# Performance work log

Measured on AMD Instinct MI355X. Metric: run time of the kernel, lower is better.

The kernel has to match this reference:

```python
import jax, jax.numpy as jnp
import numpy as np

T = 4        # number of atom types (len(atomtype))
N = 65536    # number of atoms
D = 256      # nl[0] == nl[1] == nl[2]
EPS = 1e-5   # LayerNorm eps (torch default)


def setup_inputs() -> dict:
    key = jax.random.key(0)
    ks = jax.random.split(key, 16)
    s = 1.0 / np.sqrt(D)  # xavier-ish scale
    f32 = jnp.float32
    return {
        "density": jax.random.normal(ks[0], (N, D), f32),
        "species": jax.random.randint(ks[1], (N,), 0, T, jnp.int32),
        # first Linear(nl[0], nl[1]) per type
        "W0": jax.random.normal(ks[2], (T, D, D), f32) * s,
        "b0": jnp.zeros((T, D), f32),
        # ResBlock: actfun (Relu_like: alpha*silu(Wx+b)), LayerNorm, Linear
        "Wa": jax.random.normal(ks[3], (T, D, D), f32) * s,
        "ba": jnp.zeros((T, D), f32),
        "alpha_a": jnp.ones((T, D), f32),
        "gamma": jnp.ones((T, D), f32),
        "beta_ln": jnp.zeros((T, D), f32),
        "Wl": jax.random.normal(ks[4], (T, D, D), f32) * s,
        "bl": jnp.zeros((T, D), f32),
        # tail actfun(nl[nhid-1], nl[nhid])
        "Wf": jax.random.normal(ks[5], (T, D, D), f32) * s,
        "bf": jnp.zeros((T, D), f32),
        "alpha_f": jnp.ones((T, D), f32),
        # output Linear(nl[nhid], outputneuron=1); randomized (zero-init is degenerate for testing)
        "Wo": jax.random.normal(ks[6], (T, 1, D), f32) * s,
        "bo": jnp.zeros((T, 1), f32),
    }


def _layernorm(x, g, b):
    mu = jnp.mean(x, axis=-1, keepdims=True)
    var = jnp.mean((x - mu) ** 2, axis=-1, keepdims=True)
    return g * (x - mu) * jax.lax.rsqrt(var + EPS) + b


def _expert(W0, b0, Wa, ba, alpha_a, gamma, beta_ln, Wl, bl, Wf, bf, alpha_f, Wo, bo, density):
    # Sequential: Linear -> ResBlock(actfun, LN, Linear) -> actfun -> Linear
    x = density @ W0.T + b0                       # [N, D]
    h = alpha_a * jax.nn.silu(x @ Wa.T + ba)      # Relu_like actfun
    h = _layernorm(h, gamma, beta_ln)
    x = x + (h @ Wl.T + bl)                       # residual add
    x = alpha_f * jax.nn.silu(x @ Wf.T + bf)
    return x @ Wo.T + bo                          # [N, 1]


def reference(density, species, W0, b0, Wa, ba, alpha_a, gamma, beta_ln, Wl, bl, Wf, bf, alpha_f, Wo, bo):
    # Apply every type's expert to all atoms, then pick the row for each atom's type.
    # Same math as the torch gather/scatter dispatch (every species value is in [0, T)).
    y_all = jax.vmap(_expert, in_axes=(0,) * 14 + (None,))(
        W0, b0, Wa, ba, alpha_a, gamma, beta_ln, Wl, bl, Wf, bf, alpha_f, Wo, bo, density
    )  # [T, N, 1]
    return y_all[species, jnp.arange(N)]          # [N, 1]
```

## Files before the change

kernel.cpp:

```cpp
#include <hip/hip_runtime.h>
#include <hip/hip_bf16.h>


#define D 256
#define T 4
#define MT 64
#define NTHREADS 256
#define LDSTRIDE 264

typedef __attribute__((ext_vector_type(8))) short bf16x8;
typedef __attribute__((ext_vector_type(4))) float f32x4;

__device__ __forceinline__ float bf2f(unsigned short s) {
    union { unsigned u; float f; } c;
    c.u = ((unsigned)s) << 16;
    return c.f;
}
__device__ __forceinline__ unsigned short f2bf(float f) {
    union { float f; unsigned u; } c;
    c.f = f;
    unsigned u = c.u;
    u += 0x7fffu + ((u >> 16) & 1u);
    return (unsigned short)(u >> 16);
}
__device__ __forceinline__ unsigned pack2(float a, float b) {
    return (unsigned)f2bf(a) | ((unsigned)f2bf(b) << 16);
}
__device__ __forceinline__ float lo2f(unsigned u) { return bf2f((unsigned short)(u & 0xffffu)); }
__device__ __forceinline__ float hi2f(unsigned u) { return bf2f((unsigned short)(u >> 16)); }
__device__ __forceinline__ float silu(float v) { return v / (1.f + __expf(-v)); }


extern "C" __global__ void k_hist(const int* __restrict__ species, int* counts, int N,
                                  const float* __restrict__ s0, const float* __restrict__ s1,
                                  const float* __restrict__ s2, const float* __restrict__ s3,
                                  unsigned short* __restrict__ d0, unsigned short* __restrict__ d1,
                                  unsigned short* __restrict__ d2, unsigned short* __restrict__ d3, int n4) {
    __shared__ int h[T];
    int tid = threadIdx.x;
    if (tid < T) h[tid] = 0;
    __syncthreads();
    int i = blockIdx.x * blockDim.x + tid;
    if (i < N) atomicAdd(&h[species[i]], 1);
    __syncthreads();
    if (tid < T) atomicAdd(&counts[tid], h[tid]);
    if (i < n4) {
        float4 v;
        v = ((const float4*)s0)[i];
        ((ushort4*)d0)[i] = make_ushort4(f2bf(v.x), f2bf(v.y), f2bf(v.z), f2bf(v.w));
        v = ((const float4*)s1)[i];
        ((ushort4*)d1)[i] = make_ushort4(f2bf(v.x), f2bf(v.y), f2bf(v.z), f2bf(v.w));
        v = ((const float4*)s2)[i];
        ((ushort4*)d2)[i] = make_ushort4(f2bf(v.x), f2bf(v.y), f2bf(v.z), f2bf(v.w));
        v = ((const float4*)s3)[i];
        ((ushort4*)d3)[i] = make_ushort4(f2bf(v.x), f2bf(v.y), f2bf(v.z), f2bf(v.w));
    }
}

extern "C" __global__ void k_scatter(const int* __restrict__ species, const int* __restrict__ counts,
                                     int* cursors, int* __restrict__ perm, int N) {
    __shared__ int lh[T], lbase[T];
    int tid = threadIdx.x;
    if (tid < T) lh[tid] = 0;
    __syncthreads();
    int i = blockIdx.x * blockDim.x + tid;
    int t = (i < N) ? species[i] : -1;
    int rank = 0;
    if (t >= 0) rank = atomicAdd(&lh[t], 1);
    __syncthreads();
    if (tid < T) lbase[tid] = atomicAdd(&cursors[tid], lh[tid]);
    __syncthreads();
    if (t >= 0) {
        int off = 0;
        for (int j = 0; j < t; ++j) off += counts[j];
        perm[off + lbase[t] + rank] = i;
    }
}


extern "C" __global__ void __launch_bounds__(NTHREADS, 2)
fused_moe(const float* __restrict__ density,
          const int* __restrict__ perm,
          const int* __restrict__ counts,
          const unsigned short* __restrict__ W0b,
          const unsigned short* __restrict__ Wab,
          const unsigned short* __restrict__ Wlb,
          const unsigned short* __restrict__ Wfb,
          const float* __restrict__ b0g, const float* __restrict__ bag,
          const float* __restrict__ aag, const float* __restrict__ gg,
          const float* __restrict__ btg, const float* __restrict__ blg,
          const float* __restrict__ bfg, const float* __restrict__ afg,
          const float* __restrict__ Wog, const float* __restrict__ bog,
          float* __restrict__ out, int N)
{
    __shared__ unsigned short Xs[MT * LDSTRIDE];
    __shared__ float Pb0[D], Pba[D], Paa[D], Pg[D], Pbt[D], Pbl[D], Pbf[D], Paf[D], Pwo[D];
    __shared__ float red1[NTHREADS], red2[NTHREADS];
    __shared__ float muS[MT], rsS[MT];

    const int tid = threadIdx.x;

    int c[T];
#pragma unroll
    for (int i = 0; i < T; ++i) c[i] = counts[i];
    int t = -1, tile = 0, rem = blockIdx.x, off = 0;
#pragma unroll
    for (int i = 0; i < T; ++i) {
        int ti = (c[i] + MT - 1) >> 6;
        if (t < 0) {
            if (rem < ti) { t = i; tile = rem; }
            else { rem -= ti; off += c[i]; }
        }
    }
    if (t < 0) return;
    const int bstart = off + tile * MT;
    const int nrows = min(MT, c[t] - tile * MT);

    {
        int j = t * D + tid;
        Pb0[tid] = b0g[j]; Pba[tid] = bag[j]; Paa[tid] = aag[j];
        Pg[tid]  = gg[j];  Pbt[tid] = btg[j]; Pbl[tid] = blg[j];
        Pbf[tid] = bfg[j]; Paf[tid] = afg[j]; Pwo[tid] = Wog[j];
    }

#pragma unroll
    for (int p = 0; p < 4; ++p) {
        int row = p * 16 + (tid >> 4);
        int cbase = (tid & 15) * 4;
        unsigned short* dst = Xs + row * LDSTRIDE;
        if (row < nrows) {
            const float* src = density + (size_t)perm[bstart + row] * D;
#pragma unroll
            for (int j = 0; j < 4; ++j) {
                int col = cbase + j * 64;
                float4 v = *(const float4*)(src + col);
                *(ushort4*)(dst + col) = make_ushort4(f2bf(v.x), f2bf(v.y), f2bf(v.z), f2bf(v.w));
            }
        } else {
#pragma unroll
            for (int j = 0; j < 4; ++j) {
                int col = cbase + j * 64;
                *(ushort4*)(dst + col) = make_ushort4(0, 0, 0, 0);
            }
        }
    }
    __syncthreads();

    const int lane = tid & 63;
    const int w    = tid >> 6;
    const int ml   = lane & 15;
    const int qk   = (lane >> 4) * 8;
    const int qr   = (lane >> 4) * 4;

    const size_t wmat = (size_t)t * D * D;
    const unsigned short* W0t = W0b + wmat;
    const unsigned short* Wat = Wab + wmat;
    const unsigned short* Wlt = Wlb + wmat;
    const unsigned short* Wft = Wfb + wmat;

    f32x4 acc[4][4];
    const f32x4 zero4 = {0.f, 0.f, 0.f, 0.f};

    auto do_gemm = [&](const unsigned short* __restrict__ W) {
#pragma unroll
        for (int mi = 0; mi < 4; ++mi)
#pragma unroll
            for (int ni = 0; ni < 4; ++ni) acc[mi][ni] = zero4;
#pragma unroll
        for (int k0 = 0; k0 < D; k0 += 32) {
            bf16x8 a[4], b[4];
#pragma unroll
            for (int mi = 0; mi < 4; ++mi)
                a[mi] = *(const bf16x8*)(W + (size_t)(w * 64 + mi * 16 + ml) * D + k0 + qk);
#pragma unroll
            for (int ni = 0; ni < 4; ++ni)
                b[ni] = *(const bf16x8*)(Xs + (ni * 16 + ml) * LDSTRIDE + k0 + qk);
#pragma unroll
            for (int mi = 0; mi < 4; ++mi)
#pragma unroll
                for (int ni = 0; ni < 4; ++ni)
                    acc[mi][ni] = __builtin_amdgcn_mfma_f32_16x16x32_bf16(a[mi], b[ni], acc[mi][ni], 0, 0, 0);
        }
    };


    do_gemm(W0t);
    __syncthreads();
    unsigned res[4][4][2];
#pragma unroll
    for (int mi = 0; mi < 4; ++mi) {
#pragma unroll
        for (int ni = 0; ni < 4; ++ni) {
            int r0 = w * 64 + mi * 16 + qr;
            int a0 = ni * 16 + ml;
            float4 bb = *(const float4*)(Pb0 + r0);
            float v0 = acc[mi][ni][0] + bb.x;
            float v1 = acc[mi][ni][1] + bb.y;
            float v2 = acc[mi][ni][2] + bb.z;
            float v3 = acc[mi][ni][3] + bb.w;
            res[mi][ni][0] = pack2(v0, v1);
            res[mi][ni][1] = pack2(v2, v3);
            *(ushort4*)(Xs + a0 * LDSTRIDE + r0) =
                make_ushort4(f2bf(v0), f2bf(v1), f2bf(v2), f2bf(v3));
        }
    }
    __syncthreads();

    do_gemm(Wat);
    __syncthreads();
#pragma unroll
    for (int mi = 0; mi < 4; ++mi) {
#pragma unroll
        for (int ni = 0; ni < 4; ++ni) {
            int r0 = w * 64 + mi * 16 + qr;
            int a0 = ni * 16 + ml;
            float4 bb = *(const float4*)(Pba + r0);
            float4 aa = *(const float4*)(Paa + r0);
            float v0 = aa.x * silu(acc[mi][ni][0] + bb.x);
            float v1 = aa.y * silu(acc[mi][ni][1] + bb.y);
            float v2 = aa.z * silu(acc[mi][ni][2] + bb.z);
            float v3 = aa.w * silu(acc[mi][ni][3] + bb.w);
            *(ushort4*)(Xs + a0 * LDSTRIDE + r0) =
                make_ushort4(f2bf(v0), f2bf(v1), f2bf(v2), f2bf(v3));
        }
    }
    __syncthreads();

    {
        int row = tid & 63, q = tid >> 6;
        const bf16x8* base = (const bf16x8*)(Xs + row * LDSTRIDE + q * 64);
        bf16x8 hv[8];
        float sum = 0.f, ssq = 0.f;
#pragma unroll
        for (int j = 0; j < 8; ++j) {
            hv[j] = base[j];
#pragma unroll
            for (int e = 0; e < 8; ++e) {
                float f = bf2f((unsigned short)hv[j][e]);
                sum += f; ssq += f * f;
            }
        }
        red1[tid] = sum; red2[tid] = ssq;
        __syncthreads();
        if (tid < MT) {
            float s  = red1[tid] + red1[tid + 64] + red1[tid + 128] + red1[tid + 192];
            float sq = red2[tid] + red2[tid + 64] + red2[tid + 128] + red2[tid + 192];
            float mu = s * (1.f / D);
            float var = sq * (1.f / D) - mu * mu;
            muS[tid] = mu;
            rsS[tid] = rsqrtf(var + 1e-5f);
        }
        __syncthreads();
        float mu = muS[row], rs = rsS[row];
        bf16x8* wbase = (bf16x8*)(Xs + row * LDSTRIDE + q * 64);
#pragma unroll
        for (int j = 0; j < 8; ++j) {
            bf16x8 o;
#pragma unroll
            for (int e = 0; e < 8; ++e) {
                int col = q * 64 + j * 8 + e;
                float f = bf2f((unsigned short)hv[j][e]);
                o[e] = (short)f2bf(Pg[col] * (f - mu) * rs + Pbt[col]);
            }
            wbase[j] = o;
        }
    }
    __syncthreads();

    do_gemm(Wlt);
    __syncthreads();
#pragma unroll
    for (int mi = 0; mi < 4; ++mi) {
#pragma unroll
        for (int ni = 0; ni < 4; ++ni) {
            int r0 = w * 64 + mi * 16 + qr;
            int a0 = ni * 16 + ml;
            float4 bb = *(const float4*)(Pbl + r0);
            float v0 = acc[mi][ni][0] + bb.x + lo2f(res[mi][ni][0]);
            float v1 = acc[mi][ni][1] + bb.y + hi2f(res[mi][ni][0]);
            float v2 = acc[mi][ni][2] + bb.z + lo2f(res[mi][ni][1]);
            float v3 = acc[mi][ni][3] + bb.w + hi2f(res[mi][ni][1]);
            *(ushort4*)(Xs + a0 * LDSTRIDE + r0) =
                make_ushort4(f2bf(v0), f2bf(v1), f2bf(v2), f2bf(v3));
        }
    }
    __syncthreads();

    do_gemm(Wft);
    __syncthreads();
#pragma unroll
    for (int mi = 0; mi < 4; ++mi) {
#pragma unroll
        for (int ni = 0; ni < 4; ++ni) {
            int r0 = w * 64 + mi * 16 + qr;
            int a0 = ni * 16 + ml;
            float4 bb = *(const float4*)(Pbf + r0);
            float4 aa = *(const float4*)(Paf + r0);
            float v0 = aa.x * silu(acc[mi][ni][0] + bb.x);
            float v1 = aa.y * silu(acc[mi][ni][1] + bb.y);
            float v2 = aa.z * silu(acc[mi][ni][2] + bb.z);
            float v3 = aa.w * silu(acc[mi][ni][3] + bb.w);
            *(ushort4*)(Xs + a0 * LDSTRIDE + r0) =
                make_ushort4(f2bf(v0), f2bf(v1), f2bf(v2), f2bf(v3));
        }
    }
    __syncthreads();

    {
        int row = tid & 63, q = tid >> 6;
        const bf16x8* base = (const bf16x8*)(Xs + row * LDSTRIDE + q * 64);
        float part = 0.f;
#pragma unroll
        for (int j = 0; j < 8; ++j) {
            bf16x8 hv = base[j];
#pragma unroll
            for (int e = 0; e < 8; ++e)
                part += bf2f((unsigned short)hv[e]) * Pwo[q * 64 + j * 8 + e];
        }
        red1[tid] = part;
        __syncthreads();
        if (tid < nrows) {
            float val = red1[tid] + red1[tid + 64] + red1[tid + 128] + red1[tid + 192] + bog[t];
            out[perm[bstart + tid]] = val;
        }
    }
}


extern "C" void kernel_launch(void* const* d_in, const int* in_sizes, int n_in,
                              void* d_out, int out_size, void* d_ws, size_t ws_size,
                              hipStream_t stream) {
    const float* density = (const float*)d_in[0];
    const int*   species = (const int*)d_in[1];
    const float* W0      = (const float*)d_in[2];
    const float* b0      = (const float*)d_in[3];
    const float* Wa      = (const float*)d_in[4];
    const float* ba      = (const float*)d_in[5];
    const float* alpha_a = (const float*)d_in[6];
    const float* gamma   = (const float*)d_in[7];
    const float* beta_ln = (const float*)d_in[8];
    const float* Wl      = (const float*)d_in[9];
    const float* bl      = (const float*)d_in[10];
    const float* Wf      = (const float*)d_in[11];
    const float* bfv     = (const float*)d_in[12];
    const float* alpha_f = (const float*)d_in[13];
    const float* Wo      = (const float*)d_in[14];
    const float* bo      = (const float*)d_in[15];
    float* out = (float*)d_out;
    const int N = in_sizes[1];

    char* ws = (char*)d_ws;
    int* counts  = (int*)ws;
    int* cursors = (int*)(ws + 16);
    int* perm    = (int*)(ws + 64);
    const size_t wsz = (size_t)T * D * D;
    unsigned short* W0b = (unsigned short*)(ws + 64 + (size_t)N * 4);
    unsigned short* Wab = W0b + wsz;
    unsigned short* Wlb = Wab + wsz;
    unsigned short* Wfb = Wlb + wsz;

    hipMemsetAsync(ws, 0, 32, stream);
    int n4 = (int)(wsz / 4);
    k_hist<<<(N + 255) / 256, 256, 0, stream>>>(species, counts, N, W0, Wa, Wl, Wf,
                                                W0b, Wab, Wlb, Wfb, n4);
    k_scatter<<<(N + 255) / 256, 256, 0, stream>>>(species, counts, cursors, perm, N);

    int nblocks = (N + MT - 1) / MT + T;
    fused_moe<<<nblocks, NTHREADS, 0, stream>>>(density, perm, counts, W0b, Wab, Wlb, Wfb,
                                                b0, ba, alpha_a, gamma, beta_ln, bl, bfv, alpha_f,
                                                Wo, bo, out, N);
}
```

Measured before the change: 223.1 us.

## Merge histogram and scatter into one prep kernel with per-type bucket buffers

The separate histogram and scatter kernels are replaced by a single prep kernel. It uses wavefront ballot/popcount to rank atoms within each species and appends them to fixed per-type buckets of size N, so prefix offsets from a prior count pass are no longer needed. The final cursors serve as counts for the main kernel. It also swaps the manual bf16 rounding for the hardware v_cvt_pk_bf16_f32 instruction, uses rcp in silu, and reuses two LDS parameter arrays to cut shared memory. The cost is a workspace four times larger for perm, and atom order within each bucket is no longer deterministic.

```diff
diff --git a/kernel.cpp b/kernel.cpp
--- a/kernel.cpp
+++ b/kernel.cpp
@@ -16,64 +16,48 @@
     c.u = ((unsigned)s) << 16;
     return c.f;
 }
-__device__ __forceinline__ unsigned short f2bf(float f) {
-    union { float f; unsigned u; } c;
-    c.f = f;
-    unsigned u = c.u;
-    u += 0x7fffu + ((u >> 16) & 1u);
-    return (unsigned short)(u >> 16);
-}
-__device__ __forceinline__ unsigned pack2(float a, float b) {
-    return (unsigned)f2bf(a) | ((unsigned)f2bf(b) << 16);
+__device__ __forceinline__ unsigned cvtpk(float a, float b) {
+    unsigned r;
+    asm("v_cvt_pk_bf16_f32 %0, %1, %2" : "=v"(r) : "v"(a), "v"(b));
+    return r;
 }
 __device__ __forceinline__ float lo2f(unsigned u) { return bf2f((unsigned short)(u & 0xffffu)); }
 __device__ __forceinline__ float hi2f(unsigned u) { return bf2f((unsigned short)(u >> 16)); }
-__device__ __forceinline__ float silu(float v) { return v / (1.f + __expf(-v)); }
-
-
-extern "C" __global__ void k_hist(const int* __restrict__ species, int* counts, int N,
+__device__ __forceinline__ float silu(float v) {
+    return v * __builtin_amdgcn_rcpf(1.f + __expf(-v));
+}
+
+extern "C" __global__ void k_prep(const int* __restrict__ species, int* cursors,
+                                  int* __restrict__ perm, int N,
                                   const float* __restrict__ s0, const float* __restrict__ s1,
                                   const float* __restrict__ s2, const float* __restrict__ s3,
                                   unsigned short* __restrict__ d0, unsigned short* __restrict__ d1,
                                   unsigned short* __restrict__ d2, unsigned short* __restrict__ d3, int n4) {
-    __shared__ int h[T];
-    int tid = threadIdx.x;
-    if (tid < T) h[tid] = 0;
-    __syncthreads();
-    int i = blockIdx.x * blockDim.x + tid;
-    if (i < N) atomicAdd(&h[species[i]], 1);
-    __syncthreads();
-    if (tid < T) atomicAdd(&counts[tid], h[tid]);
+    int i = blockIdx.x * blockDim.x + threadIdx.x;
     if (i < n4) {
         float4 v;
-        v = ((const float4*)s0)[i];
-        ((ushort4*)d0)[i] = make_ushort4(f2bf(v.x), f2bf(v.y), f2bf(v.z), f2bf(v.w));
-        v = ((const float4*)s1)[i];
-        ((ushort4*)d1)[i] = make_ushort4(f2bf(v.x), f2bf(v.y), f2bf(v.z), f2bf(v.w));
-        v = ((const float4*)s2)[i];
-        ((ushort4*)d2)[i] = make_ushort4(f2bf(v.x), f2bf(v.y), f2bf(v.z), f2bf(v.w));
-        v = ((const float4*)s3)[i];
-        ((ushort4*)d3)[i] = make_ushort4(f2bf(v.x), f2bf(v.y), f2bf(v.z), f2bf(v.w));
-    }
-}
-
-extern "C" __global__ void k_scatter(const int* __restrict__ species, const int* __restrict__ counts,
-                                     int* cursors, int* __restrict__ perm, int N) {
-    __shared__ int lh[T], lbase[T];
-    int tid = threadIdx.x;
-    if (tid < T) lh[tid] = 0;
-    __syncthreads();
-    int i = blockIdx.x * blockDim.x + tid;
-    int t = (i < N) ? species[i] : -1;
-    int rank = 0;
-    if (t >= 0) rank = atomicAdd(&lh[t], 1);
-    __syncthreads();
-    if (tid < T) lbase[tid] = atomicAdd(&cursors[tid], lh[tid]);
-    __syncthreads();
-    if (t >= 0) {
-        int off = 0;
-        for (int j = 0; j < t; ++j) off += counts[j];
-        perm[off + lbase[t] + rank] = i;
+        v = ((const float4*)s0)[i]; ((uint2*)d0)[i] = make_uint2(cvtpk(v.x, v.y), cvtpk(v.z, v.w));
+        v = ((const float4*)s1)[i]; ((uint2*)d1)[i] = make_uint2(cvtpk(v.x, v.y), cvtpk(v.z, v.w));
+        v = ((const float4*)s2)[i]; ((uint2*)d2)[i] = make_uint2(cvtpk(v.x, v.y), cvtpk(v.z, v.w));
+        v = ((const float4*)s3)[i]; ((uint2*)d3)[i] = make_uint2(cvtpk(v.x, v.y), cvtpk(v.z, v.w));
+    }
+    if (i < N) {
+        int t = species[i];
+        int lane = threadIdx.x & 63;
+        int idx = 0;
+#pragma unroll
+        for (int tt = 0; tt < T; ++tt) {
+            unsigned long long m = __ballot(t == tt);
+            if (t == tt) {
+                int rank = __popcll(m & ((1ull << lane) - 1ull));
+                int leader = __builtin_ctzll(m);
+                int b = 0;
+                if (lane == leader) b = atomicAdd(&cursors[tt], __popcll(m));
+                b = __shfl(b, leader, 64);
+                idx = b + rank;
+            }
+        }
+        perm[t * N + idx] = i;
     }
 }
 
@@ -94,34 +78,30 @@
           float* __restrict__ out, int N)
 {
     __shared__ unsigned short Xs[MT * LDSTRIDE];
-    __shared__ float Pb0[D], Pba[D], Paa[D], Pg[D], Pbt[D], Pbl[D], Pbf[D], Paf[D], Pwo[D];
+    __shared__ float Pbias[D], Palpha[D];
+    __shared__ float Pwo[D];
     __shared__ float red1[NTHREADS], red2[NTHREADS];
-    __shared__ float muS[MT], rsS[MT];
 
     const int tid = threadIdx.x;
 
     int c[T];
 #pragma unroll
     for (int i = 0; i < T; ++i) c[i] = counts[i];
-    int t = -1, tile = 0, rem = blockIdx.x, off = 0;
+    int t = -1, tile = 0, rem = blockIdx.x;
 #pragma unroll
     for (int i = 0; i < T; ++i) {
         int ti = (c[i] + MT - 1) >> 6;
         if (t < 0) {
             if (rem < ti) { t = i; tile = rem; }
-            else { rem -= ti; off += c[i]; }
+            else rem -= ti;
         }
     }
     if (t < 0) return;
-    const int bstart = off + tile * MT;
+    const int bstart = t * N + tile * MT;
     const int nrows = min(MT, c[t] - tile * MT);
 
-    {
-        int j = t * D + tid;
-        Pb0[tid] = b0g[j]; Pba[tid] = bag[j]; Paa[tid] = aag[j];
-        Pg[tid]  = gg[j];  Pbt[tid] = btg[j]; Pbl[tid] = blg[j];
-        Pbf[tid] = bfg[j]; Paf[tid] = afg[j]; Pwo[tid] = Wog[j];
-    }
+    Pbias[tid] = b0g[t * D + tid];
+    Pwo[tid]   = Wog[t * D + tid];
 
 #pragma unroll
     for (int p = 0; p < 4; ++p) {
@@ -134,14 +114,12 @@
             for (int j = 0; j < 4; ++j) {
                 int col = cbase + j * 64;
                 float4 v = *(const float4*)(src + col);
-                *(ushort4*)(dst + col) = make_ushort4(f2bf(v.x), f2bf(v.y), f2bf(v.z), f2bf(v.w));
+                *(uint2*)(dst + col) = make_uint2(cvtpk(v.x, v.y), cvtpk(v.z, v.w));
             }
         } else {
 #pragma unroll
-            for (int j = 0; j < 4; ++j) {
-                int col = cbase + j * 64;
-                *(ushort4*)(dst + col) = make_ushort4(0, 0, 0, 0);
-            }
+            for (int j = 0; j < 4; ++j)
+                *(uint2*)(dst + cbase + j * 64) = make_uint2(0u, 0u);
         }
     }
     __syncthreads();
@@ -193,19 +171,18 @@
         for (int ni = 0; ni < 4; ++ni) {
             int r0 = w * 64 + mi * 16 + qr;
             int a0 = ni * 16 + ml;
-            float4 bb = *(const float4*)(Pb0 + r0);
-            float v0 = acc[mi][ni][0] + bb.x;
-            float v1 = acc[mi][ni][1] + bb.y;
-            float v2 = acc[mi][ni][2] + bb.z;
-            float v3 = acc[mi][ni][3] + bb.w;
-            res[mi][ni][0] = pack2(v0, v1);
-            res[mi][ni][1] = pack2(v2, v3);
-            *(ushort4*)(Xs + a0 * LDSTRIDE + r0) =
-                make_ushort4(f2bf(v0), f2bf(v1), f2bf(v2), f2bf(v3));
-        }
-    }
-    __syncthreads();
-
+            float4 bb = *(const float4*)(Pbias + r0);
+            unsigned p01 = cvtpk(acc[mi][ni][0] + bb.x, acc[mi][ni][1] + bb.y);
+            unsigned p23 = cvtpk(acc[mi][ni][2] + bb.z, acc[mi][ni][3] + bb.w);
+            res[mi][ni][0] = p01;
+            res[mi][ni][1] = p23;
+            *(uint2*)(Xs + a0 * LDSTRIDE + r0) = make_uint2(p01, p23);
+        }
+    }
+    __syncthreads();
+
+    Pbias[tid]  = bag[t * D + tid];
+    Palpha[tid] = aag[t * D + tid];
     do_gemm(Wat);
     __syncthreads();
 #pragma unroll
@@ -214,19 +191,20 @@
         for (int ni = 0; ni < 4; ++ni) {
             int r0 = w * 64 + mi * 16 + qr;
             int a0 = ni * 16 + ml;
-            float4 bb = *(const float4*)(Pba + r0);
-            float4 aa = *(const float4*)(Paa + r0);
+            float4 bb = *(const float4*)(Pbias + r0);
+            float4 aa = *(const float4*)(Palpha + r0);
             float v0 = aa.x * silu(acc[mi][ni][0] + bb.x);
             float v1 = aa.y * silu(acc[mi][ni][1] + bb.y);
             float v2 = aa.z * silu(acc[mi][ni][2] + bb.z);
             float v3 = aa.w * silu(acc[mi][ni][3] + bb.w);
-            *(ushort4*)(Xs + a0 * LDSTRIDE + r0) =
-                make_ushort4(f2bf(v0), f2bf(v1), f2bf(v2), f2bf(v3));
+            *(uint2*)(Xs + a0 * LDSTRIDE + r0) = make_uint2(cvtpk(v0, v1), cvtpk(v2, v3));
         }
     }
     __syncthreads();
 
     {
+        Pbias[tid]  = gg[t * D + tid];
+        Palpha[tid] = btg[t * D + tid];
         int row = tid & 63, q = tid >> 6;
         const bf16x8* base = (const bf16x8*)(Xs + row * LDSTRIDE + q * 64);
         bf16x8 hv[8];
@@ -237,7 +215,8 @@
 #pragma unroll
             for (int e = 0; e < 8; ++e) {
                 float f = bf2f((unsigned short)hv[j][e]);
-                sum += f; ssq += f * f;
+                sum += f;
+                ssq = fmaf(f, f, ssq);
             }
         }
         red1[tid] = sum; red2[tid] = ssq;
@@ -247,26 +226,29 @@
             float sq = red2[tid] + red2[tid + 64] + red2[tid + 128] + red2[tid + 192];
             float mu = s * (1.f / D);
             float var = sq * (1.f / D) - mu * mu;
-            muS[tid] = mu;
-            rsS[tid] = rsqrtf(var + 1e-5f);
+            red1[tid] = mu;
+            red2[tid] = rsqrtf(var + 1e-5f);
         }
         __syncthreads();
-        float mu = muS[row], rs = rsS[row];
-        bf16x8* wbase = (bf16x8*)(Xs + row * LDSTRIDE + q * 64);
+        float mu = red1[row], rs = red2[row];
+        unsigned short* wb = Xs + row * LDSTRIDE + q * 64;
 #pragma unroll
         for (int j = 0; j < 8; ++j) {
-            bf16x8 o;
+            float n[8];
 #pragma unroll
             for (int e = 0; e < 8; ++e) {
                 int col = q * 64 + j * 8 + e;
                 float f = bf2f((unsigned short)hv[j][e]);
-                o[e] = (short)f2bf(Pg[col] * (f - mu) * rs + Pbt[col]);
+                n[e] = fmaf((f - mu) * rs, Pbias[col], Palpha[col]);
             }
-            wbase[j] = o;
-        }
-    }
-    __syncthreads();
-
+            uint4 o = make_uint4(cvtpk(n[0], n[1]), cvtpk(n[2], n[3]),
+                                 cvtpk(n[4], n[5]), cvtpk(n[6], n[7]));
+            *(uint4*)(wb + j * 8) = o;
+        }
+    }
+    __syncthreads();
+
+    Pbias[tid] = blg[t * D + tid];
     do_gemm(Wlt);
     __syncthreads();
 #pragma unroll
@@ -275,17 +257,18 @@
         for (int ni = 0; ni < 4; ++ni) {
             int r0 = w * 64 + mi * 16 + qr;
             int a0 = ni * 16 + ml;
-            float4 bb = *(const float4*)(Pbl + r0);
+            float4 bb = *(const float4*)(Pbias + r0);
             float v0 = acc[mi][ni][0] + bb.x + lo2f(res[mi][ni][0]);
             float v1 = acc[mi][ni][1] + bb.y + hi2f(res[mi][ni][0]);
             float v2 = acc[mi][ni][2] + bb.z + lo2f(res[mi][ni][1]);
             float v3 = acc[mi][ni][3] + bb.w + hi2f(res[mi][ni][1]);
-            *(ushort4*)(Xs + a0 * LDSTRIDE + r0) =
-                make_ushort4(f2bf(v0), f2bf(v1), f2bf(v2), f2bf(v3));
-        }
-    }
-    __syncthreads();
-
+            *(uint2*)(Xs + a0 * LDSTRIDE + r0) = make_uint2(cvtpk(v0, v1), cvtpk(v2, v3));
+        }
+    }
+    __syncthreads();
+
+    Pbias[tid]  = bfg[t * D + tid];
+    Palpha[tid] = afg[t * D + tid];
     do_gemm(Wft);
     __syncthreads();
 #pragma unroll
@@ -294,14 +277,13 @@
         for (int ni = 0; ni < 4; ++ni) {
             int r0 = w * 64 + mi * 16 + qr;
             int a0 = ni * 16 + ml;
-            float4 bb = *(const float4*)(Pbf + r0);
-            float4 aa = *(const float4*)(Paf + r0);
+            float4 bb = *(const float4*)(Pbias + r0);
+            float4 aa = *(const float4*)(Palpha + r0);
             float v0 = aa.x * silu(acc[mi][ni][0] + bb.x);
             float v1 = aa.y * silu(acc[mi][ni][1] + bb.y);
             float v2 = aa.z * silu(acc[mi][ni][2] + bb.z);
             float v3 = aa.w * silu(acc[mi][ni][3] + bb.w);
-            *(ushort4*)(Xs + a0 * LDSTRIDE + r0) =
-                make_ushort4(f2bf(v0), f2bf(v1), f2bf(v2), f2bf(v3));
+            *(uint2*)(Xs + a0 * LDSTRIDE + r0) = make_uint2(cvtpk(v0, v1), cvtpk(v2, v3));
         }
     }
     __syncthreads();
@@ -315,7 +297,7 @@
             bf16x8 hv = base[j];
 #pragma unroll
             for (int e = 0; e < 8; ++e)
-                part += bf2f((unsigned short)hv[e]) * Pwo[q * 64 + j * 8 + e];
+                part = fmaf(bf2f((unsigned short)hv[e]), Pwo[q * 64 + j * 8 + e], part);
         }
         red1[tid] = part;
         __syncthreads();
@@ -350,23 +332,22 @@
     const int N = in_sizes[1];
 
     char* ws = (char*)d_ws;
-    int* counts  = (int*)ws;
-    int* cursors = (int*)(ws + 16);
+    int* cursors = (int*)ws;
     int* perm    = (int*)(ws + 64);
     const size_t wsz = (size_t)T * D * D;
-    unsigned short* W0b = (unsigned short*)(ws + 64 + (size_t)N * 4);
+    unsigned short* W0b = (unsigned short*)(ws + 64 + (size_t)T * N * 4);
     unsigned short* Wab = W0b + wsz;
     unsigned short* Wlb = Wab + wsz;
     unsigned short* Wfb = Wlb + wsz;
 
-    hipMemsetAsync(ws, 0, 32, stream);
+    hipMemsetAsync(ws, 0, 16, stream);
     int n4 = (int)(wsz / 4);
-    k_hist<<<(N + 255) / 256, 256, 0, stream>>>(species, counts, N, W0, Wa, Wl, Wf,
-                                                W0b, Wab, Wlb, Wfb, n4);
-    k_scatter<<<(N + 255) / 256, 256, 0, stream>>>(species, counts, cursors, perm, N);
+    int pb = ((N > n4 ? N : n4) + 255) / 256;
+    k_prep<<<pb, 256, 0, stream>>>(species, cursors, perm, N, W0, Wa, Wl, Wf,
+                                   W0b, Wab, Wlb, Wfb, n4);
 
     int nblocks = (N + MT - 1) / MT + T;
-    fused_moe<<<nblocks, NTHREADS, 0, stream>>>(density, perm, counts, W0b, Wab, Wlb, Wfb,
+    fused_moe<<<nblocks, NTHREADS, 0, stream>>>(density, perm, cursors, W0b, Wab, Wlb, Wfb,
                                                 b0, ba, alpha_a, gamma, beta_ln, bl, bfv, alpha_f,
                                                 Wo, bo, out, N);
 }
```

Result: slower. 253.4 us (+13.6%).
